# Kernel optimization log

Hardware: AMD Instinct MI355X
Metric: run time of the kernel (lower is better)

Reference implementation:

```python
import jax, jax.numpy as jnp
import numpy as np

IN_FEATURES = 3
NUM_FREQUENCIES = 10  # in_features == 3 branch of PosEncoding
OUT_DIM = IN_FEATURES + 2 * IN_FEATURES * NUM_FREQUENCIES  # 63


def setup_inputs() -> dict:
    key = jax.random.key(0)
    coords = jax.random.uniform(key, (1, 2097152, IN_FEATURES), dtype=jnp.float32)
    return {"coords": coords}


def reference(coords) -> jnp.ndarray:
    # coords: [B, N, D] with D = IN_FEATURES
    B = coords.shape[0]
    c = coords.reshape(B, -1, IN_FEATURES)
    # freqs[i] = 2^i * pi, i = 0..NUM_FREQUENCIES-1
    freqs = (2.0 ** jnp.arange(NUM_FREQUENCIES, dtype=coords.dtype)) * jnp.pi
    # angles: [B, N, F, D]  (freq axis before feature axis to match the
    # original loop order: for i in freqs: for j in features: sin, cos)
    ang = c[:, :, None, :] * freqs[None, None, :, None]
    # [B, N, F, D, 2] -> flatten to [B, N, 2*F*D] in (i, j, sin/cos) order
    sc = jnp.stack([jnp.sin(ang), jnp.cos(ang)], axis=-1)
    sc = sc.reshape(B, c.shape[1], 2 * NUM_FREQUENCIES * IN_FEATURES)
    return jnp.concatenate([c, sc], axis=-1)  # [B, N, OUT_DIM]
```

## Files before the change

kernel.cpp:

```cpp
#include <hip/hip_runtime.h>


typedef float f32x4 __attribute__((ext_vector_type(4)));

#define BLOCK_THREADS  256
#define WAVE_PTS       64
#define OUT_PER_POINT  63
#define WAVE_FLOATS    (WAVE_PTS * OUT_PER_POINT)
#define WAVE_V4        (WAVE_FLOATS / 4)
#define BLOCK_V4       (WAVE_V4 * (BLOCK_THREADS / 64))

__global__ __launch_bounds__(BLOCK_THREADS) void posenc_kernel(
    const float* __restrict__ coords,
    f32x4* __restrict__ out4,
    int n_points)
{
    __shared__ f32x4 lds4[BLOCK_V4];
    float* lds = (float*)lds4;

    const int t    = (int)threadIdx.x;
    const int wave = t >> 6;
    const int lane = t & 63;
    const int p    = (int)blockIdx.x * BLOCK_THREADS + t;

    if (p < n_points) {
        const float c0 = coords[p * 3 + 0];
        const float c1 = coords[p * 3 + 1];
        const float c2 = coords[p * 3 + 2];

        float* o = &lds[(wave * WAVE_PTS + lane) * OUT_PER_POINT];
        o[0] = c0; o[1] = c1; o[2] = c2;

        float r0 = c0 * 0.5f, r1 = c1 * 0.5f, r2 = c2 * 0.5f;

        int k = 3;
        #pragma unroll
        for (int i = 0; i < 10; ++i) {
            const float f0 = r0 - floorf(r0);
            const float f1 = r1 - floorf(r1);
            const float f2 = r2 - floorf(r2);
            o[k + 0] = __builtin_amdgcn_sinf(f0);
            o[k + 1] = __builtin_amdgcn_cosf(f0);
            o[k + 2] = __builtin_amdgcn_sinf(f1);
            o[k + 3] = __builtin_amdgcn_cosf(f1);
            o[k + 4] = __builtin_amdgcn_sinf(f2);
            o[k + 5] = __builtin_amdgcn_cosf(f2);
            k += 6;
            r0 *= 2.0f; r1 *= 2.0f; r2 *= 2.0f;
        }
    }

    const long long gbase = (long long)blockIdx.x * BLOCK_V4 + wave * WAVE_V4;
    const long long gmax  = (long long)n_points * OUT_PER_POINT / 4;
    const int lbase = wave * WAVE_V4;

    #pragma unroll
    for (int it = 0; it < (WAVE_V4 + 63) / 64; ++it) {
        const int v = it * 64 + lane;
        if (v < WAVE_V4 && gbase + v < gmax) {
            __builtin_nontemporal_store(lds4[lbase + v], &out4[gbase + v]);
        }
    }
}

extern "C" void kernel_launch(void* const* d_in, const int* in_sizes, int n_in,
                              void* d_out, int out_size, void* d_ws, size_t ws_size,
                              hipStream_t stream) {
    const float* coords = (const float*)d_in[0];
    f32x4* out4 = (f32x4*)d_out;

    const int n_points = in_sizes[0] / 3;
    const int grid = (n_points + BLOCK_THREADS - 1) / BLOCK_THREADS;

    posenc_kernel<<<grid, BLOCK_THREADS, 0, stream>>>(coords, out4, n_points);
}
```

Baseline: 101.6 us.

## Use single-wave blocks with coalesced vector coord loads and plain stores

Shrinks blocks from four waves to one wave of 64 points and stages each block's coordinates into LDS with 16-byte vector loads instead of strided scalar loads. Output is written with regular rather than nontemporal stores, and the fast path drops per-element bounds checks. Smaller blocks raise the block count and give finer scheduling, at the cost of two barriers per block and more launch granularity. Dropping the nontemporal hint may change cache behaviour for the large write stream.

After: 99.21 us (median of 2 runs). 1.02x faster.

```diff
diff --git a/kernel.cpp b/kernel.cpp
--- a/kernel.cpp
+++ b/kernel.cpp
@@ -3,32 +3,41 @@
 
 typedef float f32x4 __attribute__((ext_vector_type(4)));
 
-#define BLOCK_THREADS  256
+#define BLOCK_THREADS  64
 #define WAVE_PTS       64
 #define OUT_PER_POINT  63
 #define WAVE_FLOATS    (WAVE_PTS * OUT_PER_POINT)
 #define WAVE_V4        (WAVE_FLOATS / 4)
-#define BLOCK_V4       (WAVE_V4 * (BLOCK_THREADS / 64))
+#define CSTAGE_V4      (WAVE_PTS * 3 / 4)
 
 __global__ __launch_bounds__(BLOCK_THREADS) void posenc_kernel(
     const float* __restrict__ coords,
     f32x4* __restrict__ out4,
     int n_points)
 {
-    __shared__ f32x4 lds4[BLOCK_V4];
-    float* lds = (float*)lds4;
+    __shared__ f32x4 tile4[WAVE_V4];
+    __shared__ f32x4 cstage4[CSTAGE_V4];
+    float* tile   = (float*)tile4;
+    float* cstage = (float*)cstage4;
 
-    const int t    = (int)threadIdx.x;
-    const int wave = t >> 6;
-    const int lane = t & 63;
-    const int p    = (int)blockIdx.x * BLOCK_THREADS + t;
+    const int lane = (int)threadIdx.x;
+    const long long pbase = (long long)blockIdx.x * WAVE_PTS;
 
-    if (p < n_points) {
-        const float c0 = coords[p * 3 + 0];
-        const float c1 = coords[p * 3 + 1];
-        const float c2 = coords[p * 3 + 2];
+    {
+        const long long in_v4 = (long long)n_points * 3 / 4;
+        const long long cb    = (long long)blockIdx.x * CSTAGE_V4;
+        if (lane < CSTAGE_V4 && cb + lane < in_v4) {
+            cstage4[lane] = ((const f32x4*)coords)[cb + lane];
+        }
+    }
+    __syncthreads();
 
-        float* o = &lds[(wave * WAVE_PTS + lane) * OUT_PER_POINT];
+    if (pbase + lane < n_points) {
+        const float c0 = cstage[lane * 3 + 0];
+        const float c1 = cstage[lane * 3 + 1];
+        const float c2 = cstage[lane * 3 + 2];
+
+        float* o = &tile[lane * OUT_PER_POINT];
         o[0] = c0; o[1] = c1; o[2] = c2;
 
         float r0 = c0 * 0.5f, r1 = c1 * 0.5f, r2 = c2 * 0.5f;
@@ -49,17 +58,20 @@
             r0 *= 2.0f; r1 *= 2.0f; r2 *= 2.0f;
         }
     }
+    __syncthreads();
 
-    const long long gbase = (long long)blockIdx.x * BLOCK_V4 + wave * WAVE_V4;
+    const long long gbase = (long long)blockIdx.x * WAVE_V4;
     const long long gmax  = (long long)n_points * OUT_PER_POINT / 4;
-    const int lbase = wave * WAVE_V4;
 
-    #pragma unroll
-    for (int it = 0; it < (WAVE_V4 + 63) / 64; ++it) {
-        const int v = it * 64 + lane;
-        if (v < WAVE_V4 && gbase + v < gmax) {
-            __builtin_nontemporal_store(lds4[lbase + v], &out4[gbase + v]);
-        }
+    if (gbase + WAVE_V4 <= gmax) {
+        #pragma unroll
+        for (int it = 0; it < WAVE_V4 / 64; ++it)
+            out4[gbase + it * 64 + lane] = tile4[it * 64 + lane];
+        if (lane < (WAVE_V4 & 63))
+            out4[gbase + (WAVE_V4 / 64) * 64 + lane] = tile4[(WAVE_V4 / 64) * 64 + lane];
+    } else {
+        for (int v = lane; v < WAVE_V4; v += 64)
+            if (gbase + v < gmax) out4[gbase + v] = tile4[v];
     }
 }
 
@@ -70,7 +82,7 @@
     f32x4* out4 = (f32x4*)d_out;
 
     const int n_points = in_sizes[0] / 3;
-    const int grid = (n_points + BLOCK_THREADS - 1) / BLOCK_THREADS;
+    const int grid = (n_points + WAVE_PTS - 1) / WAVE_PTS;
 
     posenc_kernel<<<grid, BLOCK_THREADS, 0, stream>>>(coords, out4, n_points);
 }
```
